# Optimization experiments

Measured on AMD Instinct MI355X. Metric: run time of the kernel, lower is better.

The kernel has to match this reference:

```python
import jax, jax.numpy as jnp
import numpy as np

N_NODES = 100000
N_EDGES = 1600000
IN_DIM = 128
OUT_DIM = 128
NEG_SLOPE = 0.2


def setup_inputs() -> dict:
    key = jax.random.key(0)
    ks = jax.random.split(key, 7)
    x = jax.random.normal(ks[0], (N_NODES, IN_DIM), dtype=jnp.float32)
    edge_index = jax.random.randint(ks[1], (2, N_EDGES), 0, N_NODES, dtype=jnp.int32)
    # xavier-ish scale for [in, out] weight layout (y = x @ W)
    s = float(np.sqrt(2.0 / (IN_DIM + OUT_DIM)))
    W_q = jax.random.normal(ks[2], (IN_DIM, OUT_DIM), dtype=jnp.float32) * s
    W_k = jax.random.normal(ks[3], (IN_DIM, OUT_DIM), dtype=jnp.float32) * s
    W_v = jax.random.normal(ks[4], (IN_DIM, OUT_DIM), dtype=jnp.float32) * s
    W_l = jax.random.normal(ks[5], (IN_DIM, OUT_DIM), dtype=jnp.float32) * s
    b_l = jnp.zeros((OUT_DIM,), dtype=jnp.float32)
    return {"x": x, "edge_index": edge_index, "W_q": W_q, "W_k": W_k,
            "W_v": W_v, "W_l": W_l, "b_l": b_l}


def reference(x, edge_index, W_q, W_k, W_v, W_l, b_l):
    num_nodes = x.shape[0]
    row, col = edge_index[0], edge_index[1]

    h_q = x @ W_q                                   # [N, D]
    h_k = x @ W_k                                   # [N, D]
    _h_v = x @ W_v                                  # computed in original, unused downstream

    # aggregated query: sum of neighbor queries per destination node
    q_agg = jax.ops.segment_sum(h_q[col], row, num_segments=num_nodes)  # [N, D]
    k_act = jax.nn.leaky_relu(h_k, NEG_SLOPE)

    # per-edge attention scores (note: original uses raw q_agg, not activated)
    scores = jnp.sum(k_act[row] * q_agg[col], axis=1) / (OUT_DIM ** 0.5)  # [E]

    # scatter-softmax over edges grouped by destination (row)
    max_val = jax.ops.segment_max(scores, row, num_segments=num_nodes)
    exp_scores = jnp.exp(scores - max_val[row])
    sum_exp = jax.ops.segment_sum(exp_scores, row, num_segments=num_nodes)
    alpha = exp_scores / (sum_exp[row] + 1e-8)      # [E]; dropout is identity in eval

    h_proj = x @ W_l + b_l                          # [N, D]
    weighted = alpha[:, None] * h_proj[col]         # [E, D]
    h_prime = jax.ops.segment_sum(weighted, row, num_segments=num_nodes)
    return jax.nn.leaky_relu(h_prime, NEG_SLOPE)
```

## Files before the change

kernel.cpp:

```cpp
#include <hip/hip_runtime.h>
#include <math.h>

#define N_NODES 100000
#define N_EDGES 1600000
#define DIM 128
#define CAP 64

#define NB1 196
#define NPB 512
#define CHUNK1 4096
#define GRID1 391
#define SLOT1 52
#define LSTRIDE 197

typedef short bf16x8 __attribute__((ext_vector_type(8)));
typedef float f32x4 __attribute__((ext_vector_type(4)));

static __device__ __forceinline__ unsigned bf16rne(float f) {
    unsigned u = __float_as_uint(f);
    return (u + 0x7FFFu + ((u >> 16) & 1u)) >> 16;
}
static __device__ __forceinline__ float bflo(unsigned u) { return __uint_as_float(u << 16); }
static __device__ __forceinline__ float bfhi(unsigned u) { return __uint_as_float(u & 0xFFFF0000u); }


__global__ __launch_bounds__(256) void prep_k(
    const float* __restrict__ x, const float* __restrict__ Wq,
    const float* __restrict__ Wk, const float* __restrict__ Wl,
    ushort* __restrict__ xb, ushort* __restrict__ qx, ushort* __restrict__ kactb,
    ushort* __restrict__ WqTh, ushort* __restrict__ WqTl,
    ushort* __restrict__ WlTh, ushort* __restrict__ WlTl) {
    __shared__ ushort bh[128 * 136];
    __shared__ ushort blo[128 * 136];
    int t = threadIdx.x;

    if (blockIdx.x < 2) {
        const float* W = (blockIdx.x == 0) ? Wq : Wl;
        ushort* Th = (blockIdx.x == 0) ? WqTh : WlTh;
        ushort* Tl = (blockIdx.x == 0) ? WqTl : WlTl;
        for (int i = t; i < 16384; i += 256) {
            int k = i >> 7, n = i & 127;
            float v = W[i];
            unsigned hi = bf16rne(v);
            float lo = v - bflo(hi);
            Th[n * 128 + k] = (ushort)hi;
            Tl[n * 128 + k] = (ushort)bf16rne(lo);
        }
    }
    for (int i = t; i < 16384; i += 256) {
        int k = i >> 7, n = i & 127;
        float v = Wk[i];
        unsigned hi = bf16rne(v);
        float lo = v - bflo(hi);
        bh[n * 136 + k] = (ushort)hi;
        blo[n * 136 + k] = (ushort)bf16rne(lo);
    }
    __syncthreads();

    int wave = t >> 6, lane = t & 63;
    int ln15 = lane & 15, quad = lane >> 4;
    long base = (long)blockIdx.x * 128 + wave * 32;

    bf16x8 Af[2][4];
#pragma unroll
    for (int r = 0; r < 2; r++) {
        long row = base + r * 16 + ln15;
        long rowc = row < N_NODES ? row : N_NODES - 1;
#pragma unroll
        for (int s = 0; s < 4; s++) {
            int ch = s * 4 + quad;
            const float4* xp = (const float4*)(x + rowc * 128 + ch * 8);
            float4 u0 = xp[0], u1 = xp[1];
            bf16x8 f;
            f[0] = (short)bf16rne(u0.x); f[1] = (short)bf16rne(u0.y);
            f[2] = (short)bf16rne(u0.z); f[3] = (short)bf16rne(u0.w);
            f[4] = (short)bf16rne(u1.x); f[5] = (short)bf16rne(u1.y);
            f[6] = (short)bf16rne(u1.z); f[7] = (short)bf16rne(u1.w);
            Af[r][s] = f;
            if (row < N_NODES) {
                *(bf16x8*)(xb + row * 128 + ch * 8) = f;
                uint4 fu = *(uint4*)&f;
                *(uint2*)(qx + row * 256 + 16 * ch + 4)  = make_uint2(fu.x, fu.y);
                *(uint2*)(qx + row * 256 + 16 * ch + 12) = make_uint2(fu.z, fu.w);
            }
        }
    }
    f32x4 acc[2][8];
#pragma unroll
    for (int r = 0; r < 2; r++)
#pragma unroll
        for (int t8 = 0; t8 < 8; t8++) acc[r][t8] = (f32x4){0.f, 0.f, 0.f, 0.f};
#pragma unroll
    for (int phase = 0; phase < 2; phase++) {
        const ushort* B = phase ? blo : bh;
#pragma unroll
        for (int s = 0; s < 4; s++) {
#pragma unroll
            for (int t8 = 0; t8 < 8; t8++) {
                bf16x8 b = *(const bf16x8*)(B + (t8 * 16 + ln15) * 136 + (s * 4 + quad) * 8);
                acc[0][t8] = __builtin_amdgcn_mfma_f32_16x16x32_bf16(Af[0][s], b, acc[0][t8], 0, 0, 0);
                acc[1][t8] = __builtin_amdgcn_mfma_f32_16x16x32_bf16(Af[1][s], b, acc[1][t8], 0, 0, 0);
            }
        }
    }
#pragma unroll
    for (int r = 0; r < 2; r++) {
#pragma unroll
        for (int reg = 0; reg < 4; reg++) {
            long node = base + r * 16 + quad * 4 + reg;
            if (node < N_NODES) {
#pragma unroll
                for (int t8 = 0; t8 < 8; t8++) {
                    float v = acc[r][t8][reg];
                    v = v > 0.f ? v : 0.2f * v;
                    kactb[node * 128 + t8 * 16 + ln15] = (ushort)bf16rne(v);
                }
            }
        }
    }
}


__global__ __launch_bounds__(256) void bin_k(const int* __restrict__ row,
                                             const int* __restrict__ col,
                                             unsigned* __restrict__ bkt,
                                             int* __restrict__ bktc) {
    __shared__ int lcnt[NB1];
    __shared__ unsigned lbuf[SLOT1 * LSTRIDE];
    int t = threadIdx.x, blk = blockIdx.x;
    if (t < NB1) lcnt[t] = 0;
    __syncthreads();
    long base = (long)blk * CHUNK1;
    if (base + CHUNK1 <= N_EDGES) {
        const uint4* r4 = (const uint4*)row + (size_t)blk * 1024;
        const uint4* c4 = (const uint4*)col + (size_t)blk * 1024;
#pragma unroll
        for (int q = 0; q < 4; q++) {
            uint4 rv = r4[q * 256 + t];
            uint4 cv = c4[q * 256 + t];
            unsigned rr[4] = {rv.x, rv.y, rv.z, rv.w};
            unsigned cc[4] = {cv.x, cv.y, cv.z, cv.w};
#pragma unroll
            for (int i = 0; i < 4; i++) {
                int b = rr[i] >> 9;
                int p = atomicAdd(&lcnt[b], 1);
                if (p < SLOT1) lbuf[p * LSTRIDE + b] = (cc[i] << 9) | (rr[i] & 511u);
            }
        }
    } else {
        for (int i = t; base + i < N_EDGES; i += 256) {
            unsigned r = (unsigned)row[base + i], c = (unsigned)col[base + i];
            int b = r >> 9;
            int p = atomicAdd(&lcnt[b], 1);
            if (p < SLOT1) lbuf[p * LSTRIDE + b] = (c << 9) | (r & 511u);
        }
    }
    __syncthreads();
    if (t < NB1) bktc[(size_t)blk * NB1 + t] = min(lcnt[t], SLOT1);
    int wave = t >> 6, lane = t & 63;
    for (int s = wave; s < NB1; s += 4) {
        if (lane < min(lcnt[s], SLOT1))
            bkt[((size_t)s * GRID1 + blk) * SLOT1 + lane] = lbuf[lane * LSTRIDE + s];
    }
}


__global__ __launch_bounds__(1024) void build_k(const int* __restrict__ bktc,
                                                const unsigned* __restrict__ bkt,
                                                int* __restrict__ cur,
                                                int* __restrict__ scol) {
    __shared__ int lcur[NPB];
    __shared__ int lc[GRID1];
    int b = blockIdx.x, t = threadIdx.x;
    if (t < NPB) lcur[t] = 0;
    if (t < GRID1) lc[t] = bktc[(size_t)t * NB1 + b];
    __syncthreads();
    int wave = t >> 6, lane = t & 63;
    const unsigned* D = bkt + (size_t)b * GRID1 * SLOT1;
    for (int s = wave; s < GRID1; s += 16) {
        if (lane < lc[s]) {
            unsigned v = D[(size_t)s * SLOT1 + lane];
            int rl = (int)(v & 511u);
            int c = (int)(v >> 9);
            int p = atomicAdd(&lcur[rl], 1);
            if (p < CAP) scol[((size_t)b * NPB + rl) * CAP + p] = c;
        }
    }
    __syncthreads();
    if (t < NPB) {
        int node = b * NPB + t;
        if (node < N_NODES) cur[node] = lcur[t];
    }
}


__global__ __launch_bounds__(256) void xagg_k(const uint4* __restrict__ xb4,
                                              const int* __restrict__ cur,
                                              const int* __restrict__ scol,
                                              uint4* __restrict__ xagg4) {
    int g = (blockIdx.x * 256 + threadIdx.x) >> 4;
    int gl = threadIdx.x & 15;
    int d = min(cur[g], CAP);
    float a0 = 0.f, a1 = 0.f, a2 = 0.f, a3 = 0.f;
    float a4 = 0.f, a5 = 0.f, a6 = 0.f, a7 = 0.f;
    for (int j = 0; j < d; j += 16) {
        int cb = (j + gl < d) ? scol[g * CAP + j + gl] : 0;
        int lim = min(16, d - j);
        int k = 0;
        for (; k + 4 <= lim; k += 4) {
            int c0 = __shfl(cb, k, 16),     c1 = __shfl(cb, k + 1, 16);
            int c2 = __shfl(cb, k + 2, 16), c3 = __shfl(cb, k + 3, 16);
            uint4 u0 = xb4[(size_t)c0 * 16 + gl];
            uint4 u1 = xb4[(size_t)c1 * 16 + gl];
            uint4 u2 = xb4[(size_t)c2 * 16 + gl];
            uint4 u3 = xb4[(size_t)c3 * 16 + gl];
            a0 += bflo(u0.x); a1 += bfhi(u0.x); a2 += bflo(u0.y); a3 += bfhi(u0.y);
            a4 += bflo(u0.z); a5 += bfhi(u0.z); a6 += bflo(u0.w); a7 += bfhi(u0.w);
            a0 += bflo(u1.x); a1 += bfhi(u1.x); a2 += bflo(u1.y); a3 += bfhi(u1.y);
            a4 += bflo(u1.z); a5 += bfhi(u1.z); a6 += bflo(u1.w); a7 += bfhi(u1.w);
            a0 += bflo(u2.x); a1 += bfhi(u2.x); a2 += bflo(u2.y); a3 += bfhi(u2.y);
            a4 += bflo(u2.z); a5 += bfhi(u2.z); a6 += bflo(u2.w); a7 += bfhi(u2.w);
            a0 += bflo(u3.x); a1 += bfhi(u3.x); a2 += bflo(u3.y); a3 += bfhi(u3.y);
            a4 += bflo(u3.z); a5 += bfhi(u3.z); a6 += bflo(u3.w); a7 += bfhi(u3.w);
        }
        for (; k < lim; k++) {
            int c = __shfl(cb, k, 16);
            uint4 u = xb4[(size_t)c * 16 + gl];
            a0 += bflo(u.x); a1 += bfhi(u.x); a2 += bflo(u.y); a3 += bfhi(u.y);
            a4 += bflo(u.z); a5 += bfhi(u.z); a6 += bflo(u.w); a7 += bfhi(u.w);
        }
    }
    uint4 o;
    o.x = bf16rne(a0) | (bf16rne(a1) << 16);
    o.y = bf16rne(a2) | (bf16rne(a3) << 16);
    o.z = bf16rne(a4) | (bf16rne(a5) << 16);
    o.w = bf16rne(a6) | (bf16rne(a7) << 16);
    xagg4[(size_t)g * 16 + gl] = o;
}


__global__ __launch_bounds__(256) void mgemm_k(const ushort* __restrict__ Ab,
                                               const ushort* __restrict__ BTh,
                                               const ushort* __restrict__ BTl,
                                               ushort* __restrict__ qx) {
    int tid = threadIdx.x;
    int wave = tid >> 6, lane = tid & 63;
    int ln15 = lane & 15, quad = (lane >> 4) & 3;
    long base = (long)blockIdx.x * 128 + wave * 32;

    const bf16x8* A8 = (const bf16x8*)Ab;
    const bf16x8* Bh8 = (const bf16x8*)BTh;
    const bf16x8* Bl8 = (const bf16x8*)BTl;

    bf16x8 Af[2][4];
#pragma unroll
    for (int r = 0; r < 2; r++) {
        long row = base + r * 16 + ln15;
#pragma unroll
        for (int s = 0; s < 4; s++) Af[r][s] = A8[row * 16 + s * 4 + quad];
    }
    f32x4 acc[2][8];
#pragma unroll
    for (int r = 0; r < 2; r++)
#pragma unroll
        for (int t = 0; t < 8; t++) acc[r][t] = (f32x4){0.f, 0.f, 0.f, 0.f};

#pragma unroll
    for (int phase = 0; phase < 2; phase++) {
        const bf16x8* B8 = phase ? Bl8 : Bh8;
#pragma unroll
        for (int s = 0; s < 4; s++) {
#pragma unroll
            for (int t = 0; t < 8; t++) {
                bf16x8 b = B8[(t * 16 + ln15) * 16 + s * 4 + quad];
                acc[0][t] = __builtin_amdgcn_mfma_f32_16x16x32_bf16(Af[0][s], b, acc[0][t], 0, 0, 0);
                acc[1][t] = __builtin_amdgcn_mfma_f32_16x16x32_bf16(Af[1][s], b, acc[1][t], 0, 0, 0);
            }
        }
    }
#pragma unroll
    for (int r = 0; r < 2; r++) {
#pragma unroll
        for (int reg = 0; reg < 4; reg++) {
            long node = base + r * 16 + quad * 4 + reg;
            if (node < N_NODES) {
#pragma unroll
                for (int t = 0; t < 8; t++) {
                    int j = t * 16 + ln15;
                    qx[node * 256 + (j >> 2) * 8 + (j & 3)] = (ushort)bf16rne(acc[r][t][reg]);
                }
            }
        }
    }
}


__global__ __launch_bounds__(256) void attn_k(const uint2* __restrict__ kactb,
                                              const uint4* __restrict__ qx4,
                                              const int* __restrict__ cur,
                                              const int* __restrict__ scol,
                                              uint2* __restrict__ xwb,
                                              float* __restrict__ sumw) {
    int g = (blockIdx.x * 256 + threadIdx.x) >> 5;
    int lane = threadIdx.x & 31;
    int d = min(cur[g], CAP);
    uint2 ku = kactb[(size_t)g * 32 + lane];
    const float scale = 0.08838834764831845f;
    float k0 = bflo(ku.x) * scale, k1 = bfhi(ku.x) * scale;
    float k2 = bflo(ku.y) * scale, k3 = bfhi(ku.y) * scale;

    float S = 0.f;
    float a0 = 0.f, a1 = 0.f, a2 = 0.f, a3 = 0.f;
    for (int j = 0; j < d; j += 32) {
        int cb = (j + lane < d) ? scol[g * CAP + j + lane] : 0;
        int lim = min(32, d - j);
        int k = 0;
        for (; k + 4 <= lim; k += 4) {
            int c0 = __shfl(cb, k, 32),     c1 = __shfl(cb, k + 1, 32);
            int c2 = __shfl(cb, k + 2, 32), c3 = __shfl(cb, k + 3, 32);
            uint4 u0 = qx4[(size_t)c0 * 32 + lane];
            uint4 u1 = qx4[(size_t)c1 * 32 + lane];
            uint4 u2 = qx4[(size_t)c2 * 32 + lane];
            uint4 u3 = qx4[(size_t)c3 * 32 + lane];
            float p0 = k0 * bflo(u0.x) + k1 * bfhi(u0.x) + k2 * bflo(u0.y) + k3 * bfhi(u0.y);
            float p1 = k0 * bflo(u1.x) + k1 * bfhi(u1.x) + k2 * bflo(u1.y) + k3 * bfhi(u1.y);
            float p2 = k0 * bflo(u2.x) + k1 * bfhi(u2.x) + k2 * bflo(u2.y) + k3 * bfhi(u2.y);
            float p3 = k0 * bflo(u3.x) + k1 * bfhi(u3.x) + k2 * bflo(u3.y) + k3 * bfhi(u3.y);
#pragma unroll
            for (int off = 16; off > 0; off >>= 1) {
                p0 += __shfl_xor(p0, off, 32); p1 += __shfl_xor(p1, off, 32);
                p2 += __shfl_xor(p2, off, 32); p3 += __shfl_xor(p3, off, 32);
            }
            float e0 = __expf(p0), e1 = __expf(p1);
            float e2 = __expf(p2), e3 = __expf(p3);
            S += (e0 + e1) + (e2 + e3);
            a0 += e0 * bflo(u0.z) + e1 * bflo(u1.z) + e2 * bflo(u2.z) + e3 * bflo(u3.z);
            a1 += e0 * bfhi(u0.z) + e1 * bfhi(u1.z) + e2 * bfhi(u2.z) + e3 * bfhi(u3.z);
            a2 += e0 * bflo(u0.w) + e1 * bflo(u1.w) + e2 * bflo(u2.w) + e3 * bflo(u3.w);
            a3 += e0 * bfhi(u0.w) + e1 * bfhi(u1.w) + e2 * bfhi(u2.w) + e3 * bfhi(u3.w);
        }
        for (; k < lim; k++) {
            int c = __shfl(cb, k, 32);
            uint4 u = qx4[(size_t)c * 32 + lane];
            float p = k0 * bflo(u.x) + k1 * bfhi(u.x) + k2 * bflo(u.y) + k3 * bfhi(u.y);
#pragma unroll
            for (int off = 16; off > 0; off >>= 1) p += __shfl_xor(p, off, 32);
            float e0 = __expf(p);
            S += e0;
            a0 += e0 * bflo(u.z);
            a1 += e0 * bfhi(u.z);
            a2 += e0 * bflo(u.w);
            a3 += e0 * bfhi(u.w);
        }
    }
    float inv = 1.f / (S + 1e-8f);
    uint2 o;
    o.x = bf16rne(a0 * inv) | (bf16rne(a1 * inv) << 16);
    o.y = bf16rne(a2 * inv) | (bf16rne(a3 * inv) << 16);
    xwb[(size_t)g * 32 + lane] = o;
    if (lane == 0) sumw[g] = S * inv;
}


__global__ __launch_bounds__(256) void fin_k(const ushort* __restrict__ Ab,
                                             const ushort* __restrict__ BTh,
                                             const ushort* __restrict__ BTl,
                                             const float* __restrict__ bl,
                                             const float* __restrict__ sumw,
                                             float* __restrict__ out) {
    int tid = threadIdx.x;
    int wave = tid >> 6, lane = tid & 63;
    int ln15 = lane & 15, quad = (lane >> 4) & 3;
    long base = (long)blockIdx.x * 128 + wave * 32;

    const bf16x8* A8 = (const bf16x8*)Ab;
    const bf16x8* Bh8 = (const bf16x8*)BTh;
    const bf16x8* Bl8 = (const bf16x8*)BTl;

    bf16x8 Af[2][4];
#pragma unroll
    for (int r = 0; r < 2; r++) {
        long row = base + r * 16 + ln15;
#pragma unroll
        for (int s = 0; s < 4; s++) Af[r][s] = A8[row * 16 + s * 4 + quad];
    }
    float blv[8];
#pragma unroll
    for (int t = 0; t < 8; t++) blv[t] = bl[t * 16 + ln15];

    f32x4 acc[2][8];
#pragma unroll
    for (int r = 0; r < 2; r++)
#pragma unroll
        for (int t = 0; t < 8; t++) acc[r][t] = (f32x4){0.f, 0.f, 0.f, 0.f};

#pragma unroll
    for (int phase = 0; phase < 2; phase++) {
        const bf16x8* B8 = phase ? Bl8 : Bh8;
#pragma unroll
        for (int s = 0; s < 4; s++) {
#pragma unroll
            for (int t = 0; t < 8; t++) {
                bf16x8 b = B8[(t * 16 + ln15) * 16 + s * 4 + quad];
                acc[0][t] = __builtin_amdgcn_mfma_f32_16x16x32_bf16(Af[0][s], b, acc[0][t], 0, 0, 0);
                acc[1][t] = __builtin_amdgcn_mfma_f32_16x16x32_bf16(Af[1][s], b, acc[1][t], 0, 0, 0);
            }
        }
    }
#pragma unroll
    for (int r = 0; r < 2; r++) {
#pragma unroll
        for (int reg = 0; reg < 4; reg++) {
            long node = base + r * 16 + quad * 4 + reg;
            if (node < N_NODES) {
                float sw = sumw[node];
#pragma unroll
                for (int t = 0; t < 8; t++) {
                    float v = acc[r][t][reg] + sw * blv[t];
                    v = v > 0.f ? v : 0.2f * v;
                    out[node * 128 + t * 16 + ln15] = v;
                }
            }
        }
    }
}


extern "C" void kernel_launch(void* const* d_in, const int* in_sizes, int n_in,
                              void* d_out, int out_size, void* d_ws, size_t ws_size,
                              hipStream_t stream) {
    const float* x  = (const float*)d_in[0];
    const int* row  = (const int*)d_in[1];
    const int* col  = row + N_EDGES;
    const float* Wq = (const float*)d_in[2];
    const float* Wk = (const float*)d_in[3];
    const float* Wl = (const float*)d_in[5];
    const float* bl = (const float*)d_in[6];
    float* out = (float*)d_out;

    ushort* xb    = (ushort*)d_ws;
    ushort* qx    = xb + (size_t)N_NODES * DIM;
    ushort* kactb = qx + (size_t)N_NODES * 256;
    ushort* xaggb = kactb + (size_t)N_NODES * DIM;
    ushort* xwb   = xaggb;
    unsigned* bkt = (unsigned*)xaggb;
    int* bktc     = (int*)(bkt + (size_t)NB1 * GRID1 * SLOT1);
    ushort* wbuf  = xaggb + (size_t)N_NODES * DIM;
    ushort* WqTh = wbuf,             *WqTl = wbuf + 16384;
    ushort* WlTh = wbuf + 2 * 16384, *WlTl = wbuf + 3 * 16384;
    float* sumw = (float*)(wbuf + 4 * 16384);
    int* cur  = (int*)(sumw + N_NODES);
    int* scol = cur + N_NODES;

    prep_k<<<782, 256, 0, stream>>>(x, Wq, Wk, Wl, xb, qx, kactb,
                                    WqTh, WqTl, WlTh, WlTl);
    bin_k<<<GRID1, 256, 0, stream>>>(row, col, bkt, bktc);
    build_k<<<NB1, 1024, 0, stream>>>(bktc, bkt, cur, scol);
    xagg_k<<<N_NODES / 16, 256, 0, stream>>>((const uint4*)xb, cur, scol,
                                             (uint4*)xaggb);
    mgemm_k<<<(N_NODES + 127) / 128, 256, 0, stream>>>(xaggb, WqTh, WqTl, qx);
    attn_k<<<N_NODES / 8, 256, 0, stream>>>((const uint2*)kactb, (const uint4*)qx,
                                            cur, scol, (uint2*)xwb, sumw);
    fin_k<<<(N_NODES + 127) / 128, 256, 0, stream>>>(xwb, WlTh, WlTl, bl, sumw, out);
}
```

Baseline: 486.2 us.

## Fuse neighbor aggregation with Q GEMM and attention with output GEMM

```diff
diff --git a/kernel.cpp b/kernel.cpp
--- a/kernel.cpp
+++ b/kernel.cpp
@@ -27,7 +27,7 @@
 __global__ __launch_bounds__(256) void prep_k(
     const float* __restrict__ x, const float* __restrict__ Wq,
     const float* __restrict__ Wk, const float* __restrict__ Wl,
-    ushort* __restrict__ xb, ushort* __restrict__ qx, ushort* __restrict__ kactb,
+    ushort* __restrict__ xb, ushort* __restrict__ kactb,
     ushort* __restrict__ WqTh, ushort* __restrict__ WqTl,
     ushort* __restrict__ WlTh, ushort* __restrict__ WlTl) {
     __shared__ ushort bh[128 * 136];
@@ -77,12 +77,7 @@
             f[4] = (short)bf16rne(u1.x); f[5] = (short)bf16rne(u1.y);
             f[6] = (short)bf16rne(u1.z); f[7] = (short)bf16rne(u1.w);
             Af[r][s] = f;
-            if (row < N_NODES) {
-                *(bf16x8*)(xb + row * 128 + ch * 8) = f;
-                uint4 fu = *(uint4*)&f;
-                *(uint2*)(qx + row * 256 + 16 * ch + 4)  = make_uint2(fu.x, fu.y);
-                *(uint2*)(qx + row * 256 + 16 * ch + 12) = make_uint2(fu.z, fu.w);
-            }
+            if (row < N_NODES) *(bf16x8*)(xb + row * 128 + ch * 8) = f;
         }
     }
     f32x4 acc[2][8];
@@ -194,17 +189,21 @@
 }
 
 
-__global__ __launch_bounds__(256) void xagg_k(const uint4* __restrict__ xb4,
-                                              const int* __restrict__ cur,
-                                              const int* __restrict__ scol,
-                                              uint4* __restrict__ xagg4) {
-    int g = (blockIdx.x * 256 + threadIdx.x) >> 4;
-    int gl = threadIdx.x & 15;
-    int d = min(cur[g], CAP);
+__global__ __launch_bounds__(1024) void xq_k(const uint4* __restrict__ xb4,
+                                             const int* __restrict__ cur,
+                                             const int* __restrict__ scol,
+                                             const ushort* __restrict__ BTh,
+                                             const ushort* __restrict__ BTl,
+                                             ushort* __restrict__ qb) {
+    __shared__ ushort lxa[64][136];
+    int t = threadIdx.x;
+    int g16 = t >> 4, gl = t & 15;
+    long node = (long)blockIdx.x * 64 + g16;
+    int d = (node < N_NODES) ? min(cur[node], CAP) : 0;
     float a0 = 0.f, a1 = 0.f, a2 = 0.f, a3 = 0.f;
     float a4 = 0.f, a5 = 0.f, a6 = 0.f, a7 = 0.f;
     for (int j = 0; j < d; j += 16) {
-        int cb = (j + gl < d) ? scol[g * CAP + j + gl] : 0;
+        int cb = (j + gl < d) ? scol[node * CAP + j + gl] : 0;
         int lim = min(16, d - j);
         int k = 0;
         for (; k + 4 <= lim; k += 4) {
@@ -235,76 +234,55 @@
     o.y = bf16rne(a2) | (bf16rne(a3) << 16);
     o.z = bf16rne(a4) | (bf16rne(a5) << 16);
     o.w = bf16rne(a6) | (bf16rne(a7) << 16);
-    xagg4[(size_t)g * 16 + gl] = o;
-}
-
-
-__global__ __launch_bounds__(256) void mgemm_k(const ushort* __restrict__ Ab,
+    *(uint4*)&lxa[g16][gl * 8] = o;
+    __syncthreads();
+
+    int wave = t >> 6, lane = t & 63;
+    int ln15 = lane & 15, quad = (lane >> 4) & 3;
+    const bf16x8* Bh8 = (const bf16x8*)BTh;
+    const bf16x8* Bl8 = (const bf16x8*)BTl;
+#pragma unroll
+    for (int ti = 0; ti < 2; ti++) {
+        int T = wave + ti * 16;
+        int rt = T & 3, ct = T >> 2;
+        bf16x8 af[4];
+#pragma unroll
+        for (int s = 0; s < 4; s++)
+            af[s] = *(const bf16x8*)&lxa[rt * 16 + ln15][(s * 4 + quad) * 8];
+        f32x4 acc = (f32x4){0.f, 0.f, 0.f, 0.f};
+#pragma unroll
+        for (int phase = 0; phase < 2; phase++) {
+            const bf16x8* B8 = phase ? Bl8 : Bh8;
+#pragma unroll
+            for (int s = 0; s < 4; s++)
+                acc = __builtin_amdgcn_mfma_f32_16x16x32_bf16(
+                    af[s], B8[(ct * 16 + ln15) * 16 + s * 4 + quad], acc, 0, 0, 0);
+        }
+#pragma unroll
+        for (int reg = 0; reg < 4; reg++) {
+            long n2 = (long)blockIdx.x * 64 + rt * 16 + quad * 4 + reg;
+            if (n2 < N_NODES) qb[n2 * 128 + ct * 16 + ln15] = (ushort)bf16rne(acc[reg]);
+        }
+    }
+}
+
+
+__global__ __launch_bounds__(1024) void attf_k(const uint2* __restrict__ kactb2,
+                                               const uint2* __restrict__ qb2,
+                                               const uint2* __restrict__ xb2,
+                                               const int* __restrict__ cur,
+                                               const int* __restrict__ scol,
                                                const ushort* __restrict__ BTh,
                                                const ushort* __restrict__ BTl,
-                                               ushort* __restrict__ qx) {
-    int tid = threadIdx.x;
-    int wave = tid >> 6, lane = tid & 63;
-    int ln15 = lane & 15, quad = (lane >> 4) & 3;
-    long base = (long)blockIdx.x * 128 + wave * 32;
-
-    const bf16x8* A8 = (const bf16x8*)Ab;
-    const bf16x8* Bh8 = (const bf16x8*)BTh;
-    const bf16x8* Bl8 = (const bf16x8*)BTl;
-
-    bf16x8 Af[2][4];
-#pragma unroll
-    for (int r = 0; r < 2; r++) {
-        long row = base + r * 16 + ln15;
-#pragma unroll
-        for (int s = 0; s < 4; s++) Af[r][s] = A8[row * 16 + s * 4 + quad];
-    }
-    f32x4 acc[2][8];
-#pragma unroll
-    for (int r = 0; r < 2; r++)
-#pragma unroll
-        for (int t = 0; t < 8; t++) acc[r][t] = (f32x4){0.f, 0.f, 0.f, 0.f};
-
-#pragma unroll
-    for (int phase = 0; phase < 2; phase++) {
-        const bf16x8* B8 = phase ? Bl8 : Bh8;
-#pragma unroll
-        for (int s = 0; s < 4; s++) {
-#pragma unroll
-            for (int t = 0; t < 8; t++) {
-                bf16x8 b = B8[(t * 16 + ln15) * 16 + s * 4 + quad];
-                acc[0][t] = __builtin_amdgcn_mfma_f32_16x16x32_bf16(Af[0][s], b, acc[0][t], 0, 0, 0);
-                acc[1][t] = __builtin_amdgcn_mfma_f32_16x16x32_bf16(Af[1][s], b, acc[1][t], 0, 0, 0);
-            }
-        }
-    }
-#pragma unroll
-    for (int r = 0; r < 2; r++) {
-#pragma unroll
-        for (int reg = 0; reg < 4; reg++) {
-            long node = base + r * 16 + quad * 4 + reg;
-            if (node < N_NODES) {
-#pragma unroll
-                for (int t = 0; t < 8; t++) {
-                    int j = t * 16 + ln15;
-                    qx[node * 256 + (j >> 2) * 8 + (j & 3)] = (ushort)bf16rne(acc[r][t][reg]);
-                }
-            }
-        }
-    }
-}
-
-
-__global__ __launch_bounds__(256) void attn_k(const uint2* __restrict__ kactb,
-                                              const uint4* __restrict__ qx4,
-                                              const int* __restrict__ cur,
-                                              const int* __restrict__ scol,
-                                              uint2* __restrict__ xwb,
-                                              float* __restrict__ sumw) {
-    int g = (blockIdx.x * 256 + threadIdx.x) >> 5;
-    int lane = threadIdx.x & 31;
+                                               const float* __restrict__ bl,
+                                               float* __restrict__ out) {
+    __shared__ ushort lxw[32][136];
+    __shared__ float lsw[32];
+    int t = threadIdx.x;
+    int n32 = t >> 5, lane = t & 31;
+    long g = (long)blockIdx.x * 32 + n32;
     int d = min(cur[g], CAP);
-    uint2 ku = kactb[(size_t)g * 32 + lane];
+    uint2 ku = kactb2[g * 32 + lane];
     const float scale = 0.08838834764831845f;
     float k0 = bflo(ku.x) * scale, k1 = bfhi(ku.x) * scale;
     float k2 = bflo(ku.y) * scale, k3 = bfhi(ku.y) * scale;
@@ -318,14 +296,14 @@
         for (; k + 4 <= lim; k += 4) {
             int c0 = __shfl(cb, k, 32),     c1 = __shfl(cb, k + 1, 32);
             int c2 = __shfl(cb, k + 2, 32), c3 = __shfl(cb, k + 3, 32);
-            uint4 u0 = qx4[(size_t)c0 * 32 + lane];
-            uint4 u1 = qx4[(size_t)c1 * 32 + lane];
-            uint4 u2 = qx4[(size_t)c2 * 32 + lane];
-            uint4 u3 = qx4[(size_t)c3 * 32 + lane];
-            float p0 = k0 * bflo(u0.x) + k1 * bfhi(u0.x) + k2 * bflo(u0.y) + k3 * bfhi(u0.y);
-            float p1 = k0 * bflo(u1.x) + k1 * bfhi(u1.x) + k2 * bflo(u1.y) + k3 * bfhi(u1.y);
-            float p2 = k0 * bflo(u2.x) + k1 * bfhi(u2.x) + k2 * bflo(u2.y) + k3 * bfhi(u2.y);
-            float p3 = k0 * bflo(u3.x) + k1 * bfhi(u3.x) + k2 * bflo(u3.y) + k3 * bfhi(u3.y);
+            uint2 q0 = qb2[(size_t)c0 * 32 + lane], x0 = xb2[(size_t)c0 * 32 + lane];
+            uint2 q1 = qb2[(size_t)c1 * 32 + lane], x1 = xb2[(size_t)c1 * 32 + lane];
+            uint2 q2 = qb2[(size_t)c2 * 32 + lane], x2 = xb2[(size_t)c2 * 32 + lane];
+            uint2 q3 = qb2[(size_t)c3 * 32 + lane], x3 = xb2[(size_t)c3 * 32 + lane];
+            float p0 = k0 * bflo(q0.x) + k1 * bfhi(q0.x) + k2 * bflo(q0.y) + k3 * bfhi(q0.y);
+            float p1 = k0 * bflo(q1.x) + k1 * bfhi(q1.x) + k2 * bflo(q1.y) + k3 * bfhi(q1.y);
+            float p2 = k0 * bflo(q2.x) + k1 * bfhi(q2.x) + k2 * bflo(q2.y) + k3 * bfhi(q2.y);
+            float p3 = k0 * bflo(q3.x) + k1 * bfhi(q3.x) + k2 * bflo(q3.y) + k3 * bfhi(q3.y);
 #pragma unroll
             for (int off = 16; off > 0; off >>= 1) {
                 p0 += __shfl_xor(p0, off, 32); p1 += __shfl_xor(p1, off, 32);
@@ -334,94 +312,59 @@
             float e0 = __expf(p0), e1 = __expf(p1);
             float e2 = __expf(p2), e3 = __expf(p3);
             S += (e0 + e1) + (e2 + e3);
-            a0 += e0 * bflo(u0.z) + e1 * bflo(u1.z) + e2 * bflo(u2.z) + e3 * bflo(u3.z);
-            a1 += e0 * bfhi(u0.z) + e1 * bfhi(u1.z) + e2 * bfhi(u2.z) + e3 * bfhi(u3.z);
-            a2 += e0 * bflo(u0.w) + e1 * bflo(u1.w) + e2 * bflo(u2.w) + e3 * bflo(u3.w);
-            a3 += e0 * bfhi(u0.w) + e1 * bfhi(u1.w) + e2 * bfhi(u2.w) + e3 * bfhi(u3.w);
+            a0 += e0 * bflo(x0.x) + e1 * bflo(x1.x) + e2 * bflo(x2.x) + e3 * bflo(x3.x);
+            a1 += e0 * bfhi(x0.x) + e1 * bfhi(x1.x) + e2 * bfhi(x2.x) + e3 * bfhi(x3.x);
+            a2 += e0 * bflo(x0.y) + e1 * bflo(x1.y) + e2 * bflo(x2.y) + e3 * bflo(x3.y);
+            a3 += e0 * bfhi(x0.y) + e1 * bfhi(x1.y) + e2 * bfhi(x2.y) + e3 * bfhi(x3.y);
         }
         for (; k < lim; k++) {
             int c = __shfl(cb, k, 32);
-            uint4 u = qx4[(size_t)c * 32 + lane];
-            float p = k0 * bflo(u.x) + k1 * bfhi(u.x) + k2 * bflo(u.y) + k3 * bfhi(u.y);
+            uint2 q = qb2[(size_t)c * 32 + lane], xx = xb2[(size_t)c * 32 + lane];
+            float p = k0 * bflo(q.x) + k1 * bfhi(q.x) + k2 * bflo(q.y) + k3 * bfhi(q.y);
 #pragma unroll
             for (int off = 16; off > 0; off >>= 1) p += __shfl_xor(p, off, 32);
             float e0 = __expf(p);
             S += e0;
-            a0 += e0 * bflo(u.z);
-            a1 += e0 * bfhi(u.z);
-            a2 += e0 * bflo(u.w);
-            a3 += e0 * bfhi(u.w);
+            a0 += e0 * bflo(xx.x);
+            a1 += e0 * bfhi(xx.x);
+            a2 += e0 * bflo(xx.y);
+            a3 += e0 * bfhi(xx.y);
         }
     }
     float inv = 1.f / (S + 1e-8f);
     uint2 o;
     o.x = bf16rne(a0 * inv) | (bf16rne(a1 * inv) << 16);
     o.y = bf16rne(a2 * inv) | (bf16rne(a3 * inv) << 16);
-    xwb[(size_t)g * 32 + lane] = o;
-    if (lane == 0) sumw[g] = S * inv;
-}
-
-
-__global__ __launch_bounds__(256) void fin_k(const ushort* __restrict__ Ab,
-                                             const ushort* __restrict__ BTh,
-                                             const ushort* __restrict__ BTl,
-                                             const float* __restrict__ bl,
-                                             const float* __restrict__ sumw,
-                                             float* __restrict__ out) {
-    int tid = threadIdx.x;
-    int wave = tid >> 6, lane = tid & 63;
-    int ln15 = lane & 15, quad = (lane >> 4) & 3;
-    long base = (long)blockIdx.x * 128 + wave * 32;
-
-    const bf16x8* A8 = (const bf16x8*)Ab;
+    *(uint2*)&lxw[n32][lane * 4] = o;
+    if (lane == 0) lsw[n32] = S * inv;
+    __syncthreads();
+
+    int wave = t >> 6, l64 = t & 63;
+    int ln15 = l64 & 15, quad = (l64 >> 4) & 3;
+    int rt = wave & 1, ct = wave >> 1;
     const bf16x8* Bh8 = (const bf16x8*)BTh;
     const bf16x8* Bl8 = (const bf16x8*)BTl;
-
-    bf16x8 Af[2][4];
-#pragma unroll
-    for (int r = 0; r < 2; r++) {
-        long row = base + r * 16 + ln15;
-#pragma unroll
-        for (int s = 0; s < 4; s++) Af[r][s] = A8[row * 16 + s * 4 + quad];
-    }
-    float blv[8];
-#pragma unroll
-    for (int t = 0; t < 8; t++) blv[t] = bl[t * 16 + ln15];
-
-    f32x4 acc[2][8];
-#pragma unroll
-    for (int r = 0; r < 2; r++)
-#pragma unroll
-        for (int t = 0; t < 8; t++) acc[r][t] = (f32x4){0.f, 0.f, 0.f, 0.f};
-
+    bf16x8 af[4];
+#pragma unroll
+    for (int s = 0; s < 4; s++)
+        af[s] = *(const bf16x8*)&lxw[rt * 16 + ln15][(s * 4 + quad) * 8];
+    f32x4 acc = (f32x4){0.f, 0.f, 0.f, 0.f};
 #pragma unroll
     for (int phase = 0; phase < 2; phase++) {
         const bf16x8* B8 = phase ? Bl8 : Bh8;
 #pragma unroll
-        for (int s = 0; s < 4; s++) {
-#pragma unroll
-            for (int t = 0; t < 8; t++) {
-                bf16x8 b = B8[(t * 16 + ln15) * 16 + s * 4 + quad];
-                acc[0][t] = __builtin_amdgcn_mfma_f32_16x16x32_bf16(Af[0][s], b, acc[0][t], 0, 0, 0);
-                acc[1][t] = __builtin_amdgcn_mfma_f32_16x16x32_bf16(Af[1][s], b, acc[1][t], 0, 0, 0);
-            }
-        }
-    }
-#pragma unroll
-    for (int r = 0; r < 2; r++) {
-#pragma unroll
-        for (int reg = 0; reg < 4; reg++) {
-            long node = base + r * 16 + quad * 4 + reg;
-            if (node < N_NODES) {
-                float sw = sumw[node];
-#pragma unroll
-                for (int t = 0; t < 8; t++) {
-                    float v = acc[r][t][reg] + sw * blv[t];
-                    v = v > 0.f ? v : 0.2f * v;
-                    out[node * 128 + t * 16 + ln15] = v;
-                }
-            }
-        }
+        for (int s = 0; s < 4; s++)
+            acc = __builtin_amdgcn_mfma_f32_16x16x32_bf16(
+                af[s], B8[(ct * 16 + ln15) * 16 + s * 4 + quad], acc, 0, 0, 0);
+    }
+    float blv = bl[ct * 16 + ln15];
+#pragma unroll
+    for (int reg = 0; reg < 4; reg++) {
+        int rrow = rt * 16 + quad * 4 + reg;
+        long node = (long)blockIdx.x * 32 + rrow;
+        float v = acc[reg] + lsw[rrow] * blv;
+        v = v > 0.f ? v : 0.2f * v;
+        out[node * 128 + ct * 16 + ln15] = v;
     }
 }
 
@@ -439,27 +382,23 @@
     float* out = (float*)d_out;
 
     ushort* xb    = (ushort*)d_ws;
-    ushort* qx    = xb + (size_t)N_NODES * DIM;
-    ushort* kactb = qx + (size_t)N_NODES * 256;
-    ushort* xaggb = kactb + (size_t)N_NODES * DIM;
-    ushort* xwb   = xaggb;
-    unsigned* bkt = (unsigned*)xaggb;
-    int* bktc     = (int*)(bkt + (size_t)NB1 * GRID1 * SLOT1);
-    ushort* wbuf  = xaggb + (size_t)N_NODES * DIM;
+    ushort* qb    = xb + (size_t)N_NODES * DIM;
+    ushort* kactb = qb + (size_t)N_NODES * DIM;
+    ushort* wbuf  = kactb + (size_t)N_NODES * DIM;
     ushort* WqTh = wbuf,             *WqTl = wbuf + 16384;
     ushort* WlTh = wbuf + 2 * 16384, *WlTl = wbuf + 3 * 16384;
-    float* sumw = (float*)(wbuf + 4 * 16384);
-    int* cur  = (int*)(sumw + N_NODES);
+    int* cur  = (int*)(wbuf + 4 * 16384);
     int* scol = cur + N_NODES;
-
-    prep_k<<<782, 256, 0, stream>>>(x, Wq, Wk, Wl, xb, qx, kactb,
+    unsigned* bkt = (unsigned*)(scol + (size_t)N_NODES * CAP);
+    int* bktc = (int*)(bkt + (size_t)NB1 * GRID1 * SLOT1);
+
+    prep_k<<<782, 256, 0, stream>>>(x, Wq, Wk, Wl, xb, kactb,
                                     WqTh, WqTl, WlTh, WlTl);
     bin_k<<<GRID1, 256, 0, stream>>>(row, col, bkt, bktc);
     build_k<<<NB1, 1024, 0, stream>>>(bktc, bkt, cur, scol);
-    xagg_k<<<N_NODES / 16, 256, 0, stream>>>((const uint4*)xb, cur, scol,
-                                             (uint4*)xaggb);
-    mgemm_k<<<(N_NODES + 127) / 128, 256, 0, stream>>>(xaggb, WqTh, WqTl, qx);
-    attn_k<<<N_NODES / 8, 256, 0, stream>>>((const uint2*)kactb, (const uint4*)qx,
-                                            cur, scol, (uint2*)xwb, sumw);
-    fin_k<<<(N_NODES + 127) / 128, 256, 0, stream>>>(xwb, WlTh, WlTl, bl, sumw, out);
-}
+    xq_k<<<(N_NODES + 63) / 64, 1024, 0, stream>>>((const uint4*)xb, cur, scol,
+                                                   WqTh, WqTl, qb);
+    attf_k<<<N_NODES / 32, 1024, 0, stream>>>((const uint2*)kactb, (const uint2*)qb,
+                                              (const uint2*)xb, cur, scol,
+                                              WlTh, WlTl, bl, out);
+}
```

New measurement: 470.3 us. 1.03x faster.

## Fuse neighbor aggregation with Wq GEMM via shared-memory staging

Applied to the files above, without the earlier changes.

```diff
diff --git a/kernel.cpp b/kernel.cpp
--- a/kernel.cpp
+++ b/kernel.cpp
@@ -194,17 +194,21 @@
 }
 
 
-__global__ __launch_bounds__(256) void xagg_k(const uint4* __restrict__ xb4,
-                                              const int* __restrict__ cur,
-                                              const int* __restrict__ scol,
-                                              uint4* __restrict__ xagg4) {
-    int g = (blockIdx.x * 256 + threadIdx.x) >> 4;
-    int gl = threadIdx.x & 15;
-    int d = min(cur[g], CAP);
+__global__ __launch_bounds__(1024) void xq_k(const uint4* __restrict__ xb4,
+                                             const int* __restrict__ cur,
+                                             const int* __restrict__ scol,
+                                             const ushort* __restrict__ BTh,
+                                             const ushort* __restrict__ BTl,
+                                             ushort* __restrict__ qx) {
+    __shared__ ushort lxa[64][136];
+    int t = threadIdx.x;
+    int g16 = t >> 4, gl = t & 15;
+    long node = (long)blockIdx.x * 64 + g16;
+    int d = (node < N_NODES) ? min(cur[node], CAP) : 0;
     float a0 = 0.f, a1 = 0.f, a2 = 0.f, a3 = 0.f;
     float a4 = 0.f, a5 = 0.f, a6 = 0.f, a7 = 0.f;
     for (int j = 0; j < d; j += 16) {
-        int cb = (j + gl < d) ? scol[g * CAP + j + gl] : 0;
+        int cb = (j + gl < d) ? scol[node * CAP + j + gl] : 0;
         int lim = min(16, d - j);
         int k = 0;
         for (; k + 4 <= lim; k += 4) {
@@ -235,60 +239,36 @@
     o.y = bf16rne(a2) | (bf16rne(a3) << 16);
     o.z = bf16rne(a4) | (bf16rne(a5) << 16);
     o.w = bf16rne(a6) | (bf16rne(a7) << 16);
-    xagg4[(size_t)g * 16 + gl] = o;
-}
-
-
-__global__ __launch_bounds__(256) void mgemm_k(const ushort* __restrict__ Ab,
-                                               const ushort* __restrict__ BTh,
-                                               const ushort* __restrict__ BTl,
-                                               ushort* __restrict__ qx) {
-    int tid = threadIdx.x;
-    int wave = tid >> 6, lane = tid & 63;
+    *(uint4*)&lxa[g16][gl * 8] = o;
+    __syncthreads();
+
+    int wave = t >> 6, lane = t & 63;
     int ln15 = lane & 15, quad = (lane >> 4) & 3;
-    long base = (long)blockIdx.x * 128 + wave * 32;
-
-    const bf16x8* A8 = (const bf16x8*)Ab;
     const bf16x8* Bh8 = (const bf16x8*)BTh;
     const bf16x8* Bl8 = (const bf16x8*)BTl;
-
-    bf16x8 Af[2][4];
-#pragma unroll
-    for (int r = 0; r < 2; r++) {
-        long row = base + r * 16 + ln15;
-#pragma unroll
-        for (int s = 0; s < 4; s++) Af[r][s] = A8[row * 16 + s * 4 + quad];
-    }
-    f32x4 acc[2][8];
-#pragma unroll
-    for (int r = 0; r < 2; r++)
-#pragma unroll
-        for (int t = 0; t < 8; t++) acc[r][t] = (f32x4){0.f, 0.f, 0.f, 0.f};
-
-#pragma unroll
-    for (int phase = 0; phase < 2; phase++) {
-        const bf16x8* B8 = phase ? Bl8 : Bh8;
-#pragma unroll
-        for (int s = 0; s < 4; s++) {
-#pragma unroll
-            for (int t = 0; t < 8; t++) {
-                bf16x8 b = B8[(t * 16 + ln15) * 16 + s * 4 + quad];
-                acc[0][t] = __builtin_amdgcn_mfma_f32_16x16x32_bf16(Af[0][s], b, acc[0][t], 0, 0, 0);
-                acc[1][t] = __builtin_amdgcn_mfma_f32_16x16x32_bf16(Af[1][s], b, acc[1][t], 0, 0, 0);
-            }
-        }
-    }
-#pragma unroll
-    for (int r = 0; r < 2; r++) {
+#pragma unroll
+    for (int ti = 0; ti < 2; ti++) {
+        int T = wave + ti * 16;
+        int rt = T & 3, ct = T >> 2;
+        bf16x8 af[4];
+#pragma unroll
+        for (int s = 0; s < 4; s++)
+            af[s] = *(const bf16x8*)&lxa[rt * 16 + ln15][(s * 4 + quad) * 8];
+        f32x4 acc = (f32x4){0.f, 0.f, 0.f, 0.f};
+#pragma unroll
+        for (int phase = 0; phase < 2; phase++) {
+            const bf16x8* B8 = phase ? Bl8 : Bh8;
+#pragma unroll
+            for (int s = 0; s < 4; s++)
+                acc = __builtin_amdgcn_mfma_f32_16x16x32_bf16(
+                    af[s], B8[(ct * 16 + ln15) * 16 + s * 4 + quad], acc, 0, 0, 0);
+        }
 #pragma unroll
         for (int reg = 0; reg < 4; reg++) {
-            long node = base + r * 16 + quad * 4 + reg;
-            if (node < N_NODES) {
-#pragma unroll
-                for (int t = 0; t < 8; t++) {
-                    int j = t * 16 + ln15;
-                    qx[node * 256 + (j >> 2) * 8 + (j & 3)] = (ushort)bf16rne(acc[r][t][reg]);
-                }
+            long n2 = (long)blockIdx.x * 64 + rt * 16 + quad * 4 + reg;
+            if (n2 < N_NODES) {
+                int j = ct * 16 + ln15;
+                qx[n2 * 256 + (j >> 2) * 8 + (j & 3)] = (ushort)bf16rne(acc[reg]);
             }
         }
     }
@@ -441,24 +421,22 @@
     ushort* xb    = (ushort*)d_ws;
     ushort* qx    = xb + (size_t)N_NODES * DIM;
     ushort* kactb = qx + (size_t)N_NODES * 256;
-    ushort* xaggb = kactb + (size_t)N_NODES * DIM;
-    ushort* xwb   = xaggb;
-    unsigned* bkt = (unsigned*)xaggb;
-    int* bktc     = (int*)(bkt + (size_t)NB1 * GRID1 * SLOT1);
-    ushort* wbuf  = xaggb + (size_t)N_NODES * DIM;
+    ushort* xwb   = kactb + (size_t)N_NODES * DIM;
+    ushort* wbuf  = xwb + (size_t)N_NODES * DIM;
     ushort* WqTh = wbuf,             *WqTl = wbuf + 16384;
     ushort* WlTh = wbuf + 2 * 16384, *WlTl = wbuf + 3 * 16384;
     float* sumw = (float*)(wbuf + 4 * 16384);
     int* cur  = (int*)(sumw + N_NODES);
     int* scol = cur + N_NODES;
+    unsigned* bkt = (unsigned*)(scol + (size_t)N_NODES * CAP);
+    int* bktc = (int*)(bkt + (size_t)NB1 * GRID1 * SLOT1);
 
     prep_k<<<782, 256, 0, stream>>>(x, Wq, Wk, Wl, xb, qx, kactb,
                                     WqTh, WqTl, WlTh, WlTl);
     bin_k<<<GRID1, 256, 0, stream>>>(row, col, bkt, bktc);
     build_k<<<NB1, 1024, 0, stream>>>(bktc, bkt, cur, scol);
-    xagg_k<<<N_NODES / 16, 256, 0, stream>>>((const uint4*)xb, cur, scol,
-                                             (uint4*)xaggb);
-    mgemm_k<<<(N_NODES + 127) / 128, 256, 0, stream>>>(xaggb, WqTh, WqTl, qx);
+    xq_k<<<(N_NODES + 63) / 64, 1024, 0, stream>>>((const uint4*)xb, cur, scol,
+                                                   WqTh, WqTl, qx);
     attn_k<<<N_NODES / 8, 256, 0, stream>>>((const uint2*)kactb, (const uint4*)qx,
                                             cur, scol, (uint2*)xwb, sumw);
     fin_k<<<(N_NODES + 127) / 128, 256, 0, stream>>>(xwb, WlTh, WlTl, bl, sumw, out);
```

Result: slower. 496.5 us (+2.1%).
